# Performance work log

Measured on AMD Instinct MI355X. Metric: run time of the kernel, lower is better.

## Reference

```python
import jax, jax.numpy as jnp
import numpy as np

N, E, B = 10000, 20000, 400
ND, ED, D = 32, 16, 64


def setup_inputs() -> dict:
    key = jax.random.key(0)
    ks = jax.random.split(key, 32)

    def lin(k, out_d, in_d):
        kw, kb = jax.random.split(k)
        s = 1.0 / np.sqrt(in_d)
        return (jax.random.uniform(kw, (out_d, in_d), jnp.float32, -s, s),
                jax.random.uniform(kb, (out_d,), jnp.float32, -s, s))

    W_in, b_in = lin(ks[0], D, ND)
    W_e1, b_e1 = lin(ks[1], D, ED)
    W_e2, b_e2 = lin(ks[2], D * D, D)
    b_conv = jax.random.uniform(ks[3], (D,), jnp.float32, -1/8.0, 1/8.0)
    W_ih, b_ih = lin(ks[4], 3 * D, D)
    W_hh, b_hh = lin(ks[5], 3 * D, D)
    W_ih_l, b_ih_l = lin(ks[6], 4 * D, 2 * D)
    W_hh_l, b_hh_l = lin(ks[7], 4 * D, D)
    W_o1, b_o1 = lin(ks[8], D, 2 * D)
    W_o2, b_o2 = lin(ks[9], 1, D)

    x = jax.random.normal(ks[10], (N, ND), jnp.float32)
    edge_attr = jax.random.normal(ks[11], (E, ED), jnp.float32)
    edge_index = jax.random.randint(ks[12], (2, E), 0, N, jnp.int64)
    batch = jnp.sort(jax.random.randint(ks[13], (N,), 0, B, jnp.int64))

    return dict(x=x, edge_attr=edge_attr,
                W_in=W_in, b_in=b_in, W_e1=W_e1, b_e1=b_e1, W_e2=W_e2, b_e2=b_e2,
                b_conv=b_conv, W_ih=W_ih, b_ih=b_ih, W_hh=W_hh, b_hh=b_hh,
                W_ih_l=W_ih_l, b_ih_l=b_ih_l, W_hh_l=W_hh_l, b_hh_l=b_hh_l,
                W_o1=W_o1, b_o1=b_o1, W_o2=W_o2, b_o2=b_o2,
                edge_index=edge_index, batch=batch)


def reference(x, edge_attr, W_in, b_in, W_e1, b_e1, W_e2, b_e2, b_conv,
              W_ih, b_ih, W_hh, b_hh, W_ih_l, b_ih_l, W_hh_l, b_hh_l,
              W_o1, b_o1, W_o2, b_o2, edge_index, batch):
    src, dst = edge_index[0], edge_index[1]

    # in_linear
    out = jax.nn.relu(x @ W_in.T + b_in)            # [N, D]
    h = out                                          # GRU hidden (layer=1, seq=1)

    # edge-conditioned weights: MLP(edge_attr) -> [E, D, D]
    ew = (jax.nn.relu(edge_attr @ W_e1.T + b_e1) @ W_e2.T + b_e2).reshape(E, D, D)
    cnt = jnp.maximum(jax.ops.segment_sum(jnp.ones((E,), x.dtype), dst, N), 1.0)

    for _ in range(3):
        # NNConv: gather src nodes, per-edge matmul, scatter-mean to dst, + bias
        msg = jnp.einsum('ed,edf->ef', out[src], ew)                 # [E, D]
        agg = jax.ops.segment_sum(msg, dst, N) / cnt[:, None] + b_conv
        m = jax.nn.relu(agg)
        # GRU cell (torch gate order r, z, n)
        gi = m @ W_ih.T + b_ih
        gh = h @ W_hh.T + b_hh
        i_r, i_z, i_n = jnp.split(gi, 3, axis=-1)
        h_r, h_z, h_n = jnp.split(gh, 3, axis=-1)
        r = jax.nn.sigmoid(i_r + h_r)
        z = jax.nn.sigmoid(i_z + h_z)
        n = jnp.tanh(i_n + r * h_n)
        h = (1.0 - z) * n + z * h
        out = h

    # Set2Set pooling, processing_steps=3
    q_star = jnp.zeros((B, 2 * D), x.dtype)
    hl = jnp.zeros((B, D), x.dtype)
    cl = jnp.zeros((B, D), x.dtype)
    for _ in range(3):
        g = q_star @ W_ih_l.T + b_ih_l + hl @ W_hh_l.T + b_hh_l
        gi_, gf_, gg_, go_ = jnp.split(g, 4, axis=-1)   # torch order i,f,g,o
        cl = jax.nn.sigmoid(gf_) * cl + jax.nn.sigmoid(gi_) * jnp.tanh(gg_)
        hl = jax.nn.sigmoid(go_) * jnp.tanh(cl)
        q = hl                                           # [B, D]
        e = jnp.sum(out * q[batch], axis=-1)             # [N]
        mmax = jax.ops.segment_max(e, batch, B)
        a = jnp.exp(e - mmax[batch])
        a = a / jax.ops.segment_sum(a, batch, B)[batch]
        r_ = jax.ops.segment_sum(a[:, None] * out, batch, B)  # [B, D]
        q_star = jnp.concatenate([q, r_], axis=-1)

    o = jax.nn.relu(q_star @ W_o1.T + b_o1) @ W_o2.T + b_o2
    return o.reshape(-1)
```

## Files before the change

kernel.cpp:

```cpp
#include <hip/hip_runtime.h>
#include <math.h>


#define Nn 10000
#define Ee 20000
#define Bb 400
#define KSTEPS 130
#define S2S_CHUNK 1024

typedef __attribute__((ext_vector_type(8))) short bf16x8_t;
typedef __attribute__((ext_vector_type(4))) float f32x4_t;

__device__ __forceinline__ float sigmoidf_(float x) { return 1.f / (1.f + expf(-x)); }

__device__ __forceinline__ void split8(const float* p, bf16x8_t& Ahi_, bf16x8_t& Alo_) {
    union { bf16x8_t v; unsigned u[4]; } hi, lo;
#pragma unroll
    for (int ii = 0; ii < 4; ++ii) {
        float pa = p[2 * ii], pb = p[2 * ii + 1];
        unsigned ua = __float_as_uint(pa), ub = __float_as_uint(pb);
        hi.u[ii] = (ua >> 16) | (ub & 0xFFFF0000u);
        float la = pa - __uint_as_float(ua & 0xFFFF0000u);
        float lb = pb - __uint_as_float(ub & 0xFFFF0000u);
        lo.u[ii] = (__float_as_uint(la) >> 16) | (__float_as_uint(lb) & 0xFFFF0000u);
    }
    Ahi_ = hi.v; Alo_ = lo.v;
}

__global__ __launch_bounds__(256) void k_in_linear(const float* __restrict__ x,
                                                   const float* __restrict__ Win,
                                                   const float* __restrict__ bin,
                                                   float* __restrict__ out) {
    int idx = blockIdx.x * 256 + threadIdx.x;
    if (idx >= Nn * 64) return;
    int n = idx >> 6, j = idx & 63;
    const float* xr = x + n * 32;
    const float* w = Win + j * 32;
    float acc = bin[j];
#pragma unroll
    for (int k = 0; k < 32; ++k) acc += xr[k] * w[k];
    out[idx] = fmaxf(acc, 0.f);
}

__global__ __launch_bounds__(256) void k_edge_mlp1(const float* __restrict__ ea,
                                                   const float* __restrict__ W1,
                                                   const float* __restrict__ b1,
                                                   const int* __restrict__ epos,
                                                   float* __restrict__ eh) {
    int idx = blockIdx.x * 256 + threadIdx.x;
    if (idx >= Ee * 64) return;
    int e = idx >> 6, j = idx & 63;
    const float* ar = ea + e * 16;
    const float* w = W1 + j * 16;
    float acc = b1[j];
#pragma unroll
    for (int k = 0; k < 16; ++k) acc += ar[k] * w[k];
    eh[(size_t)epos[e] * 64 + j] = fmaxf(acc, 0.f);
}

__global__ __launch_bounds__(256) void k_make_Bfat(const float* __restrict__ W2,
                                                   const float* __restrict__ b2,
                                                   unsigned short* __restrict__ Bfat) {
    int idx = blockIdx.x * 256 + threadIdx.x;
    if (idx >= KSTEPS * 4096) return;
    int i  = idx & 7;
    int l  = (idx >> 3) & 63;
    int nq = (idx >> 9) & 3;
    int h  = (idx >> 11) & 1;
    int ks = idx >> 12;
    int kap = ks * 32 + (l >> 4) * 8 + i;
    int f = nq * 16 + (l & 15);
    float w;
    if (kap < 4096) {
        int q = kap >> 6, d = kap & 63;
        w = W2[(size_t)(d * 64 + f) * 64 + q];
    } else {
        int d = kap - 4096;
        w = b2[d * 64 + f];
    }
    unsigned u = __float_as_uint(w);
    unsigned short outv;
    if (h == 0) {
        outv = (unsigned short)(u >> 16);
    } else {
        float lo = w - __uint_as_float(u & 0xFFFF0000u);
        outv = (unsigned short)(__float_as_uint(lo) >> 16);
    }
    Bfat[idx] = outv;
}

__global__ __launch_bounds__(256) void k_make_Wg(const float* __restrict__ Wih,
                                                 const float* __restrict__ Whh,
                                                 unsigned short* __restrict__ Wg) {
    int idx = blockIdx.x * 256 + threadIdx.x;
    if (idx >= 4 * 2 * 16 * 64 * 8) return;
    int i  = idx & 7;
    int l  = (idx >> 3) & 63;
    int t  = (idx >> 9) & 15;
    int h  = (idx >> 13) & 1;
    int ks = idx >> 14;
    int k = ks * 32 + (l >> 4) * 8 + i;
    int u = t * 16 + (l & 15);
    int j = u & 63, part = u >> 6;
    float w = 0.f;
    if (part == 0) w = (k < 64) ? Wih[(size_t)j * 64 + k]          : Whh[(size_t)j * 64 + (k - 64)];
    if (part == 1) w = (k < 64) ? Wih[(size_t)(64 + j) * 64 + k]   : Whh[(size_t)(64 + j) * 64 + (k - 64)];
    if (part == 2) w = (k < 64) ? Wih[(size_t)(128 + j) * 64 + k]  : 0.f;
    if (part == 3) w = (k < 64) ? 0.f : Whh[(size_t)(128 + j) * 64 + (k - 64)];
    unsigned uu = __float_as_uint(w);
    unsigned short outv;
    if (h == 0) {
        outv = (unsigned short)(uu >> 16);
    } else {
        float lo = w - __uint_as_float(uu & 0xFFFF0000u);
        outv = (unsigned short)(__float_as_uint(lo) >> 16);
    }
    Wg[idx] = outv;
}

__global__ __launch_bounds__(256) void k_count_deg(const int* __restrict__ ei,
                                                   int* __restrict__ deg) {
    int e = blockIdx.x * 256 + threadIdx.x;
    if (e >= Ee) return;
    atomicAdd(&deg[ei[Ee + e]], 1);
}

__global__ __launch_bounds__(256) void k_scan_nodes(const int* __restrict__ deg,
                                                    int* __restrict__ rowptr,
                                                    int* __restrict__ wptr) {
    __shared__ int part[256];
    int t = threadIdx.x;
    const int PER = (Nn + 255) / 256;
    int b0 = t * PER;
    int s = 0;
    for (int i = 0; i < PER; ++i) {
        int idx = b0 + i;
        if (idx < Nn) s += deg[idx];
    }
    part[t] = s;
    __syncthreads();
    for (int o = 1; o < 256; o <<= 1) {
        int u = (t >= o) ? part[t - o] : 0;
        __syncthreads();
        part[t] += u;
        __syncthreads();
    }
    int run = part[t] - s;
    for (int i = 0; i < PER; ++i) {
        int idx = b0 + i;
        if (idx < Nn) {
            rowptr[idx] = run;
            wptr[idx] = run;
            run += deg[idx];
        }
    }
    if (t == 255) rowptr[Nn] = run;
}

__global__ __launch_bounds__(256) void k_sort_edges(const int* __restrict__ ei,
                                                    int* __restrict__ wptr,
                                                    int* __restrict__ srcs,
                                                    int* __restrict__ epos) {
    int e = blockIdx.x * 256 + threadIdx.x;
    if (e >= Ee) return;
    int d = ei[Ee + e];
    int p = atomicAdd(&wptr[d], 1);
    srcs[p] = ei[e];
    epos[e] = p;
}

__global__ __launch_bounds__(256, 3) void k_msg_mfma(const float* __restrict__ out,
                                                     const float* __restrict__ eh,
                                                     const unsigned short* __restrict__ Bfat,
                                                     const int* __restrict__ srcs_g,
                                                     float* __restrict__ msgbuf,
                                                     int nsplit) {
    __shared__ float ehs[128][20];
    __shared__ int srcs[128];
    int tid = threadIdx.x;
    int ebase = blockIdx.x * 128;
    int ksplit = blockIdx.y;

    int ks0 = (KSTEPS * ksplit) / nsplit;
    int ks1 = (KSTEPS * (ksplit + 1)) / nsplit;
    int q0 = ks0 >> 1;
    int qn = ((min(ks1, 128) - 1) >> 1) - q0 + 1;

    {
        int el = tid >> 1, seg = tid & 1;
        int eg = ebase + el;
        bool v = eg < Ee;
        if (seg == 0) srcs[el] = v ? srcs_g[eg] : 0;
        const float* erow = eh + (size_t)eg * 64;
        for (int j = seg; j < qn; j += 2)
            ehs[el][j] = v ? erow[q0 + j] : 0.f;
    }
    __syncthreads();

    int lane = tid & 63;
    int wtile = tid >> 6;
    int m16 = lane & 15;
    int g = lane >> 4;
    int erA = wtile * 32 + m16;
    int erB = erA + 16;

    float a0[2][8], a1[2][8];
    {
        const float* rA = out + (size_t)srcs[erA] * 64;
        const float* rB = out + (size_t)srcs[erB] * 64;
        float4 v0, v1;
        v0 = *(const float4*)(rA + g * 8);      v1 = *(const float4*)(rA + g * 8 + 4);
        a0[0][0]=v0.x; a0[0][1]=v0.y; a0[0][2]=v0.z; a0[0][3]=v0.w;
        a0[0][4]=v1.x; a0[0][5]=v1.y; a0[0][6]=v1.z; a0[0][7]=v1.w;
        v0 = *(const float4*)(rA + 32 + g * 8); v1 = *(const float4*)(rA + 36 + g * 8);
        a1[0][0]=v0.x; a1[0][1]=v0.y; a1[0][2]=v0.z; a1[0][3]=v0.w;
        a1[0][4]=v1.x; a1[0][5]=v1.y; a1[0][6]=v1.z; a1[0][7]=v1.w;
        v0 = *(const float4*)(rB + g * 8);      v1 = *(const float4*)(rB + g * 8 + 4);
        a0[1][0]=v0.x; a0[1][1]=v0.y; a0[1][2]=v0.z; a0[1][3]=v0.w;
        a0[1][4]=v1.x; a0[1][5]=v1.y; a0[1][6]=v1.z; a0[1][7]=v1.w;
        v0 = *(const float4*)(rB + 32 + g * 8); v1 = *(const float4*)(rB + 36 + g * 8);
        a1[1][0]=v0.x; a1[1][1]=v0.y; a1[1][2]=v0.z; a1[1][3]=v0.w;
        a1[1][4]=v1.x; a1[1][5]=v1.y; a1[1][6]=v1.z; a1[1][7]=v1.w;
    }

    f32x4_t acc[2][4];
#pragma unroll
    for (int t = 0; t < 2; ++t)
#pragma unroll
        for (int nq = 0; nq < 4; ++nq) acc[t][nq] = (f32x4_t){0.f, 0.f, 0.f, 0.f};

    auto body = [&](int ks, const float (&Av)[2][8], float qA, float qB) {
        const unsigned short* bstep = Bfat + (size_t)ks * 4096;
        bf16x8_t bhi[4], blo[4];
#pragma unroll
        for (int nq = 0; nq < 4; ++nq) {
            bhi[nq] = *(const bf16x8_t*)(bstep + ((size_t)(nq * 64 + lane)) * 8);
            blo[nq] = *(const bf16x8_t*)(bstep + ((size_t)((4 + nq) * 64 + lane)) * 8);
        }
        float pA[8], pB[8];
#pragma unroll
        for (int i = 0; i < 8; ++i) { pA[i] = Av[0][i] * qA; pB[i] = Av[1][i] * qB; }
        bf16x8_t AhiA, AloA, AhiB, AloB;
        split8(pA, AhiA, AloA);
        split8(pB, AhiB, AloB);
#pragma unroll
        for (int nq = 0; nq < 4; ++nq) {
            acc[0][nq] = __builtin_amdgcn_mfma_f32_16x16x32_bf16(AhiA, bhi[nq], acc[0][nq], 0, 0, 0);
            acc[0][nq] = __builtin_amdgcn_mfma_f32_16x16x32_bf16(AhiA, blo[nq], acc[0][nq], 0, 0, 0);
            acc[0][nq] = __builtin_amdgcn_mfma_f32_16x16x32_bf16(AloA, bhi[nq], acc[0][nq], 0, 0, 0);
            acc[1][nq] = __builtin_amdgcn_mfma_f32_16x16x32_bf16(AhiB, bhi[nq], acc[1][nq], 0, 0, 0);
            acc[1][nq] = __builtin_amdgcn_mfma_f32_16x16x32_bf16(AhiB, blo[nq], acc[1][nq], 0, 0, 0);
            acc[1][nq] = __builtin_amdgcn_mfma_f32_16x16x32_bf16(AloB, bhi[nq], acc[1][nq], 0, 0, 0);
        }
    };

    for (int kp = ks0 & ~1; kp < ks1; kp += 2) {
        float qA = 1.f, qB = 1.f;
        if (kp < 128) {
            int qi = (kp >> 1) - q0;
            if (qi >= 0) { qA = ehs[erA][qi]; qB = ehs[erB][qi]; }
        }
        if (kp >= ks0)    body(kp,     a0, qA, qB);
        if (kp + 1 < ks1) body(kp + 1, a1, qA, qB);
    }

#pragma unroll
    for (int t = 0; t < 2; ++t) {
#pragma unroll
        for (int r = 0; r < 4; ++r) {
            int el = wtile * 32 + t * 16 + g * 4 + r;
            int eg = ebase + el;
            if (eg >= Ee) continue;
            float* mrow = msgbuf + ((size_t)ksplit * Ee + eg) * 64 + m16;
#pragma unroll
            for (int nq = 0; nq < 4; ++nq)
                mrow[nq * 16] = acc[t][nq][r];
        }
    }
}

__global__ __launch_bounds__(256) void k_gru_mfma(const float* __restrict__ msgbuf,
                                                  const int* __restrict__ rowptr,
                                                  const float* __restrict__ bconv,
                                                  const unsigned short* __restrict__ Wg,
                                                  const float* __restrict__ bih,
                                                  const float* __restrict__ bhh,
                                                  float* __restrict__ out,
                                                  int nsplit) {
    __shared__ float ms[64][68];
    __shared__ float hs[64][68];
    int tid = threadIdx.x;
    int nbase = blockIdx.x * 64;

    {
        int nl = tid >> 2, seg = tid & 3;
        int ng = nbase + nl;
        bool v = ng < Nn;
        int p0 = v ? rowptr[ng] : 0;
        int p1 = v ? rowptr[ng + 1] : 0;
        int dg = p1 - p0;
        float rc = 1.f / (float)(dg < 1 ? 1 : dg);
        float s[16];
#pragma unroll
        for (int i = 0; i < 16; ++i) s[i] = 0.f;
        for (int sp = 0; sp < nsplit; ++sp) {
            const float* mb = msgbuf + (size_t)sp * Ee * 64;
            for (int p = p0; p < p1; ++p) {
                const float* mrow = mb + (size_t)p * 64 + seg * 16;
#pragma unroll
                for (int c4 = 0; c4 < 4; ++c4) {
                    float4 t4 = *(const float4*)(mrow + c4 * 4);
                    s[c4 * 4 + 0] += t4.x;
                    s[c4 * 4 + 1] += t4.y;
                    s[c4 * 4 + 2] += t4.z;
                    s[c4 * 4 + 3] += t4.w;
                }
            }
        }
        const float* hrow = out + (size_t)ng * 64 + seg * 16;
        float4 z = make_float4(0.f, 0.f, 0.f, 0.f);
#pragma unroll
        for (int c4 = 0; c4 < 4; ++c4) {
            int col = seg * 16 + c4 * 4;
            float4 hv = v ? *(const float4*)(hrow + c4 * 4) : z;
            ms[nl][col + 0] = fmaxf(s[c4 * 4 + 0] * rc + bconv[col + 0], 0.f);
            ms[nl][col + 1] = fmaxf(s[c4 * 4 + 1] * rc + bconv[col + 1], 0.f);
            ms[nl][col + 2] = fmaxf(s[c4 * 4 + 2] * rc + bconv[col + 2], 0.f);
            ms[nl][col + 3] = fmaxf(s[c4 * 4 + 3] * rc + bconv[col + 3], 0.f);
            *(float4*)&hs[nl][col] = hv;
        }
    }
    __syncthreads();

    int lane = tid & 63;
    int wtile = tid >> 6;
    int m16 = lane & 15;
    int g = lane >> 4;
    int er = wtile * 16 + m16;

    f32x4_t acc[16];
#pragma unroll
    for (int t = 0; t < 16; ++t) acc[t] = (f32x4_t){0.f, 0.f, 0.f, 0.f};

#pragma unroll
    for (int ks = 0; ks < 4; ++ks) {
        const float* src = (ks < 2) ? &ms[er][ks * 32 + g * 8]
                                    : &hs[er][(ks - 2) * 32 + g * 8];
        float p[8];
#pragma unroll
        for (int ii = 0; ii < 8; ++ii) p[ii] = src[ii];
        bf16x8_t Ahi, Alo;
        split8(p, Ahi, Alo);
        const unsigned short* bstep = Wg + (size_t)ks * (2 * 16 * 512);
#pragma unroll
        for (int t = 0; t < 16; ++t) {
            bf16x8_t bhi = *(const bf16x8_t*)(bstep + ((size_t)t * 64 + lane) * 8);
            bf16x8_t blo = *(const bf16x8_t*)(bstep + ((size_t)(16 + t) * 64 + lane) * 8);
            acc[t] = __builtin_amdgcn_mfma_f32_16x16x32_bf16(Ahi, bhi, acc[t], 0, 0, 0);
            acc[t] = __builtin_amdgcn_mfma_f32_16x16x32_bf16(Ahi, blo, acc[t], 0, 0, 0);
            acc[t] = __builtin_amdgcn_mfma_f32_16x16x32_bf16(Alo, bhi, acc[t], 0, 0, 0);
        }
    }

#pragma unroll
    for (int t2 = 0; t2 < 4; ++t2) {
        int jj = t2 * 16 + m16;
        float br = bih[jj] + bhh[jj];
        float bz = bih[64 + jj] + bhh[64 + jj];
        float bin_ = bih[128 + jj];
        float bhn = bhh[128 + jj];
#pragma unroll
        for (int r = 0; r < 4; ++r) {
            int nl2 = wtile * 16 + g * 4 + r;
            int ng2 = nbase + nl2;
            if (ng2 >= Nn) continue;
            float rg = sigmoidf_(acc[t2][r] + br);
            float z  = sigmoidf_(acc[4 + t2][r] + bz);
            float nn = tanhf(acc[8 + t2][r] + bin_ + rg * (acc[12 + t2][r] + bhn));
            float hv = hs[nl2][jj];
            out[(size_t)ng2 * 64 + jj] = (1.f - z) * nn + z * hv;
        }
    }
}

__global__ __launch_bounds__(256) void k_count_batch(const int* __restrict__ batch,
                                                     int* __restrict__ bcount) {
    int n = blockIdx.x * 256 + threadIdx.x;
    if (n >= Nn) return;
    atomicAdd(&bcount[batch[n]], 1);
}

__global__ __launch_bounds__(64) void k_scan_batch(const int* __restrict__ bcount,
                                                   int* __restrict__ bstart) {
    int lane = threadIdx.x;
    const int PER = (Bb + 63) / 64;
    int base = lane * PER;
    int v[PER];
    int s = 0;
#pragma unroll
    for (int i = 0; i < PER; ++i) {
        int idx = base + i;
        int c = (idx < Bb) ? bcount[idx] : 0;
        v[i] = s;
        s += c;
    }
    int inc = s;
#pragma unroll
    for (int o = 1; o < 64; o <<= 1) {
        int t = __shfl_up(inc, o, 64);
        if (lane >= o) inc += t;
    }
    int excl = inc - s;
    int total = __shfl(inc, 63, 64);
#pragma unroll
    for (int i = 0; i < PER; ++i) {
        int idx = base + i;
        if (idx < Bb) bstart[idx] = excl + v[i];
    }
    if (lane == 63) bstart[Bb] = total;
}

__device__ __forceinline__ float block_reduce_max_(float v, float* red, int tid) {
#pragma unroll
    for (int o = 32; o; o >>= 1) v = fmaxf(v, __shfl_xor(v, o, 64));
    if ((tid & 63) == 0) red[tid >> 6] = v;
    __syncthreads();
    float r = fmaxf(fmaxf(red[0], red[1]), fmaxf(red[2], red[3]));
    __syncthreads();
    return r;
}
__device__ __forceinline__ float block_reduce_sum_(float v, float* red, int tid) {
#pragma unroll
    for (int o = 32; o; o >>= 1) v += __shfl_xor(v, o, 64);
    if ((tid & 63) == 0) red[tid >> 6] = v;
    __syncthreads();
    float r = (red[0] + red[1]) + (red[2] + red[3]);
    __syncthreads();
    return r;
}

__global__ __launch_bounds__(256) void k_set2set(const float* __restrict__ out,
                                                 const int* __restrict__ bstart,
                                                 const float* __restrict__ Wil,
                                                 const float* __restrict__ bil,
                                                 const float* __restrict__ Whl,
                                                 const float* __restrict__ bhl,
                                                 const float* __restrict__ Wo1,
                                                 const float* __restrict__ bo1,
                                                 const float* __restrict__ Wo2,
                                                 const float* __restrict__ bo2,
                                                 float* __restrict__ outp) {
    __shared__ float qs[128];
    __shared__ float hs2[64];
    __shared__ float cs[64];
    __shared__ float g_lds[256];
    __shared__ float e_lds[S2S_CHUNK];
    __shared__ float red[4];
    __shared__ float rpart[4][64];

    int b = blockIdx.x, tid = threadIdx.x;
    int lane = tid & 63, wv = tid >> 6;
    int s = bstart[b], eend = bstart[b + 1];
    int cntb = eend - s;

    if (tid < 128) qs[tid] = 0.f;
    if (tid < 64) { hs2[tid] = 0.f; cs[tid] = 0.f; }
    __syncthreads();

    for (int step = 0; step < 3; ++step) {
        {
            int u = tid;
            float acc = bil[u] + bhl[u];
            const float4* wi = (const float4*)(Wil + (size_t)u * 128);
#pragma unroll
            for (int k4 = 0; k4 < 32; ++k4) {
                float4 w = wi[k4];
                acc += qs[k4 * 4 + 0] * w.x + qs[k4 * 4 + 1] * w.y +
                       qs[k4 * 4 + 2] * w.z + qs[k4 * 4 + 3] * w.w;
            }
            const float4* wh = (const float4*)(Whl + (size_t)u * 64);
#pragma unroll
            for (int k4 = 0; k4 < 16; ++k4) {
                float4 w = wh[k4];
                acc += hs2[k4 * 4 + 0] * w.x + hs2[k4 * 4 + 1] * w.y +
                       hs2[k4 * 4 + 2] * w.z + hs2[k4 * 4 + 3] * w.w;
            }
            g_lds[u] = acc;
        }
        __syncthreads();
        if (tid < 64) {
            float c = sigmoidf_(g_lds[64 + tid]) * cs[tid] +
                      sigmoidf_(g_lds[tid]) * tanhf(g_lds[128 + tid]);
            cs[tid] = c;
            float h = sigmoidf_(g_lds[192 + tid]) * tanhf(c);
            hs2[tid] = h;
            qs[tid] = h;
        }
        __syncthreads();

        float gmax = -INFINITY, gsum = 0.f, racc = 0.f;
        for (int c0 = s; c0 < eend; c0 += S2S_CHUNK) {
            int clen = min(S2S_CHUNK, eend - c0);
            for (int i = tid; i < clen; i += 256) {
                const float4* orow = (const float4*)(out + (size_t)(c0 + i) * 64);
                float a0 = 0.f, a1 = 0.f, a2 = 0.f, a3 = 0.f;
#pragma unroll
                for (int k4 = 0; k4 < 16; k4 += 4) {
                    float4 o0 = orow[k4], o1 = orow[k4 + 1], o2 = orow[k4 + 2], o3 = orow[k4 + 3];
                    a0 += o0.x * qs[k4 * 4 + 0]  + o0.y * qs[k4 * 4 + 1]  + o0.z * qs[k4 * 4 + 2]  + o0.w * qs[k4 * 4 + 3];
                    a1 += o1.x * qs[k4 * 4 + 4]  + o1.y * qs[k4 * 4 + 5]  + o1.z * qs[k4 * 4 + 6]  + o1.w * qs[k4 * 4 + 7];
                    a2 += o2.x * qs[k4 * 4 + 8]  + o2.y * qs[k4 * 4 + 9]  + o2.z * qs[k4 * 4 + 10] + o2.w * qs[k4 * 4 + 11];
                    a3 += o3.x * qs[k4 * 4 + 12] + o3.y * qs[k4 * 4 + 13] + o3.z * qs[k4 * 4 + 14] + o3.w * qs[k4 * 4 + 15];
                }
                e_lds[i] = (a0 + a1) + (a2 + a3);
            }
            __syncthreads();
            float m = -INFINITY;
            for (int i = tid; i < clen; i += 256) m = fmaxf(m, e_lds[i]);
            float cmax = block_reduce_max_(m, red, tid);
            float nm = fmaxf(gmax, cmax);
            float scale = expf(gmax - nm);
            gsum *= scale; racc *= scale;
            float lsum = 0.f;
            for (int i = tid; i < clen; i += 256) {
                float av = expf(e_lds[i] - nm);
                e_lds[i] = av;
                lsum += av;
            }
            gsum += block_reduce_sum_(lsum, red, tid);
            for (int i = wv; i < clen; i += 4)
                racc += e_lds[i] * out[(size_t)(c0 + i) * 64 + lane];
            gmax = nm;
            __syncthreads();
        }
        rpart[wv][lane] = racc;
        __syncthreads();
        if (tid < 64) {
            float r = (rpart[0][tid] + rpart[1][tid]) + (rpart[2][tid] + rpart[3][tid]);
            qs[64 + tid] = (cntb > 0) ? r / gsum : 0.f;
        }
        __syncthreads();
    }

    if (tid < 64) {
        float acc = bo1[tid];
        const float4* w = (const float4*)(Wo1 + (size_t)tid * 128);
#pragma unroll
        for (int k4 = 0; k4 < 32; ++k4) {
            float4 wv4 = w[k4];
            acc += qs[k4 * 4 + 0] * wv4.x + qs[k4 * 4 + 1] * wv4.y +
                   qs[k4 * 4 + 2] * wv4.z + qs[k4 * 4 + 3] * wv4.w;
        }
        acc = fmaxf(acc, 0.f);
        float t = acc * Wo2[tid];
#pragma unroll
        for (int o = 32; o; o >>= 1) t += __shfl_xor(t, o, 64);
        if (tid == 0) outp[b] = t + bo2[0];
    }
}

extern "C" void kernel_launch(void* const* d_in, const int* in_sizes, int n_in,
                              void* d_out, int out_size, void* d_ws, size_t ws_size,
                              hipStream_t stream) {
    const float* x        = (const float*)d_in[0];
    const float* ea       = (const float*)d_in[1];
    const float* W_in     = (const float*)d_in[2];
    const float* b_in     = (const float*)d_in[3];
    const float* W_e1     = (const float*)d_in[4];
    const float* b_e1     = (const float*)d_in[5];
    const float* W_e2     = (const float*)d_in[6];
    const float* b_e2     = (const float*)d_in[7];
    const float* b_conv   = (const float*)d_in[8];
    const float* W_ih     = (const float*)d_in[9];
    const float* b_ih     = (const float*)d_in[10];
    const float* W_hh     = (const float*)d_in[11];
    const float* b_hh     = (const float*)d_in[12];
    const float* W_ih_l   = (const float*)d_in[13];
    const float* b_ih_l   = (const float*)d_in[14];
    const float* W_hh_l   = (const float*)d_in[15];
    const float* b_hh_l   = (const float*)d_in[16];
    const float* W_o1     = (const float*)d_in[17];
    const float* b_o1     = (const float*)d_in[18];
    const float* W_o2     = (const float*)d_in[19];
    const float* b_o2     = (const float*)d_in[20];
    const int*   ei       = (const int*)d_in[21];
    const int*   batch    = (const int*)d_in[22];
    float* outp = (float*)d_out;

    char* base = (char*)d_ws;
    size_t off = 0;
    auto carve = [&](size_t bytes) -> void* {
        void* p = base + off;
        off = (off + bytes + 255) & ~(size_t)255;
        return p;
    };

    int ns = 4;
    float *out, *msgbuf, *eh;
    unsigned short *Bfat, *Wg;
    int *srcs, *epos, *rowptr, *wptr, *deg, *bcount, *bstart;
    for (;; ns >>= 1) {
        off = 0;
        out    = (float*)carve((size_t)Nn * 64 * 4);
        msgbuf = (float*)carve((size_t)ns * Ee * 64 * 4);
        eh     = (float*)carve((size_t)Ee * 64 * 4);
        Bfat   = (unsigned short*)carve((size_t)KSTEPS * 4096 * 2);
        Wg     = (unsigned short*)carve((size_t)4 * 2 * 16 * 64 * 8 * 2);
        srcs   = (int*)carve((size_t)Ee * 4);
        epos   = (int*)carve((size_t)Ee * 4);
        rowptr = (int*)carve((size_t)(Nn + 1) * 4);
        wptr   = (int*)carve((size_t)Nn * 4);
        deg    = (int*)carve((size_t)Nn * 4);
        bcount = (int*)carve((size_t)Bb * 4);
        bstart = (int*)carve((size_t)(Bb + 1) * 4);
        if (off <= ws_size || ns == 1) break;
    }
    if (off > ws_size) return;

    hipMemsetAsync(deg, 0, (size_t)Nn * 4, stream);
    hipMemsetAsync(bcount, 0, (size_t)Bb * 4, stream);

    k_count_deg<<<(Ee + 255) / 256, 256, 0, stream>>>(ei, deg);
    k_scan_nodes<<<1, 256, 0, stream>>>(deg, rowptr, wptr);
    k_sort_edges<<<(Ee + 255) / 256, 256, 0, stream>>>(ei, wptr, srcs, epos);

    k_in_linear<<<(Nn * 64) / 256, 256, 0, stream>>>(x, W_in, b_in, out);
    k_edge_mlp1<<<(Ee * 64) / 256, 256, 0, stream>>>(ea, W_e1, b_e1, epos, eh);
    k_make_Bfat<<<(KSTEPS * 4096) / 256, 256, 0, stream>>>(W_e2, b_e2, Bfat);
    k_make_Wg<<<(4 * 2 * 16 * 64 * 8) / 256, 256, 0, stream>>>(W_ih, W_hh, Wg);
    k_count_batch<<<(Nn + 255) / 256, 256, 0, stream>>>(batch, bcount);
    k_scan_batch<<<1, 64, 0, stream>>>(bcount, bstart);

    int eblocks = (Ee + 127) / 128;
    int nblocks = (Nn + 63) / 64;
    for (int it = 0; it < 3; ++it) {
        k_msg_mfma<<<dim3(eblocks, ns), 256, 0, stream>>>(out, eh, Bfat, srcs, msgbuf, ns);
        k_gru_mfma<<<nblocks, 256, 0, stream>>>(msgbuf, rowptr, b_conv, Wg, b_ih, b_hh, out, ns);
    }

    k_set2set<<<Bb, 256, 0, stream>>>(out, bstart, W_ih_l, b_ih_l, W_hh_l, b_hh_l,
                                      W_o1, b_o1, W_o2, b_o2, outp);
}
```

Before: 340.2 us.

## Merge setup kernels and double-buffer B fragment loads in message kernel

Merges the in-linear, Bfat and Wg preparation kernels into one fill launch, and combines degree/batch counting and their scans into paired kernels, cutting the number of small serial launches. Separately, the message MFMA kernel now prefetches the next k-step's B fragments into registers while the current step computes, and its occupancy hint in launch_bounds is removed. The prefetch raises register pressure, and dropping the occupancy hint may let the compiler lower occupancy.

Result: faster. 332.8 us (-2.2%).

```diff
diff --git a/kernel.cpp b/kernel.cpp
--- a/kernel.cpp
+++ b/kernel.cpp
@@ -7,6 +7,10 @@
 #define Bb 400
 #define KSTEPS 130
 #define S2S_CHUNK 1024
+
+#define FILL_A (Nn * 64)
+#define FILL_B (KSTEPS * 4096)
+#define FILL_C (4 * 2 * 16 * 64 * 8)
 
 typedef __attribute__((ext_vector_type(8))) short bf16x8_t;
 typedef __attribute__((ext_vector_type(4))) float f32x4_t;
@@ -27,19 +31,80 @@
     Ahi_ = hi.v; Alo_ = lo.v;
 }
 
-__global__ __launch_bounds__(256) void k_in_linear(const float* __restrict__ x,
-                                                   const float* __restrict__ Win,
-                                                   const float* __restrict__ bin,
-                                                   float* __restrict__ out) {
+__global__ __launch_bounds__(256) void k_fill(const float* __restrict__ x,
+                                              const float* __restrict__ Win,
+                                              const float* __restrict__ bin,
+                                              const float* __restrict__ W2,
+                                              const float* __restrict__ b2,
+                                              const float* __restrict__ Wih,
+                                              const float* __restrict__ Whh,
+                                              float* __restrict__ out,
+                                              unsigned short* __restrict__ Bfat,
+                                              unsigned short* __restrict__ Wg) {
     int idx = blockIdx.x * 256 + threadIdx.x;
-    if (idx >= Nn * 64) return;
-    int n = idx >> 6, j = idx & 63;
-    const float* xr = x + n * 32;
-    const float* w = Win + j * 32;
-    float acc = bin[j];
-#pragma unroll
-    for (int k = 0; k < 32; ++k) acc += xr[k] * w[k];
-    out[idx] = fmaxf(acc, 0.f);
+    if (idx < FILL_A) {
+        int n = idx >> 6, j = idx & 63;
+        const float* xr = x + n * 32;
+        const float* w = Win + j * 32;
+        float acc = bin[j];
+#pragma unroll
+        for (int k = 0; k < 32; ++k) acc += xr[k] * w[k];
+        out[idx] = fmaxf(acc, 0.f);
+        return;
+    }
+    idx -= FILL_A;
+    if (idx < FILL_B) {
+        int i  = idx & 7;
+        int l  = (idx >> 3) & 63;
+        int nq = (idx >> 9) & 3;
+        int h  = (idx >> 11) & 1;
+        int ks = idx >> 12;
+        int kap = ks * 32 + (l >> 4) * 8 + i;
+        int f = nq * 16 + (l & 15);
+        float w;
+        if (kap < 4096) {
+            int q = kap >> 6, d = kap & 63;
+            w = W2[(size_t)(d * 64 + f) * 64 + q];
+        } else {
+            int d = kap - 4096;
+            w = b2[d * 64 + f];
+        }
+        unsigned u = __float_as_uint(w);
+        unsigned short outv;
+        if (h == 0) {
+            outv = (unsigned short)(u >> 16);
+        } else {
+            float lo = w - __uint_as_float(u & 0xFFFF0000u);
+            outv = (unsigned short)(__float_as_uint(lo) >> 16);
+        }
+        Bfat[idx] = outv;
+        return;
+    }
+    idx -= FILL_B;
+    if (idx < FILL_C) {
+        int i  = idx & 7;
+        int l  = (idx >> 3) & 63;
+        int t  = (idx >> 9) & 15;
+        int h  = (idx >> 13) & 1;
+        int ks = idx >> 14;
+        int k = ks * 32 + (l >> 4) * 8 + i;
+        int u = t * 16 + (l & 15);
+        int j = u & 63, part = u >> 6;
+        float w = 0.f;
+        if (part == 0) w = (k < 64) ? Wih[(size_t)j * 64 + k]          : Whh[(size_t)j * 64 + (k - 64)];
+        if (part == 1) w = (k < 64) ? Wih[(size_t)(64 + j) * 64 + k]   : Whh[(size_t)(64 + j) * 64 + (k - 64)];
+        if (part == 2) w = (k < 64) ? Wih[(size_t)(128 + j) * 64 + k]  : 0.f;
+        if (part == 3) w = (k < 64) ? 0.f : Whh[(size_t)(128 + j) * 64 + (k - 64)];
+        unsigned uu = __float_as_uint(w);
+        unsigned short outv;
+        if (h == 0) {
+            outv = (unsigned short)(uu >> 16);
+        } else {
+            float lo = w - __uint_as_float(uu & 0xFFFF0000u);
+            outv = (unsigned short)(__float_as_uint(lo) >> 16);
+        }
+        Wg[idx] = outv;
+    }
 }
 
 __global__ __launch_bounds__(256) void k_edge_mlp1(const float* __restrict__ ea,
@@ -58,103 +123,79 @@
     eh[(size_t)epos[e] * 64 + j] = fmaxf(acc, 0.f);
 }
 
-__global__ __launch_bounds__(256) void k_make_Bfat(const float* __restrict__ W2,
-                                                   const float* __restrict__ b2,
-                                                   unsigned short* __restrict__ Bfat) {
+__global__ __launch_bounds__(256) void k_prep_count(const int* __restrict__ ei,
+                                                    const int* __restrict__ batch,
+                                                    int* __restrict__ deg,
+                                                    int* __restrict__ bcount) {
     int idx = blockIdx.x * 256 + threadIdx.x;
-    if (idx >= KSTEPS * 4096) return;
-    int i  = idx & 7;
-    int l  = (idx >> 3) & 63;
-    int nq = (idx >> 9) & 3;
-    int h  = (idx >> 11) & 1;
-    int ks = idx >> 12;
-    int kap = ks * 32 + (l >> 4) * 8 + i;
-    int f = nq * 16 + (l & 15);
-    float w;
-    if (kap < 4096) {
-        int q = kap >> 6, d = kap & 63;
-        w = W2[(size_t)(d * 64 + f) * 64 + q];
-    } else {
-        int d = kap - 4096;
-        w = b2[d * 64 + f];
-    }
-    unsigned u = __float_as_uint(w);
-    unsigned short outv;
-    if (h == 0) {
-        outv = (unsigned short)(u >> 16);
-    } else {
-        float lo = w - __uint_as_float(u & 0xFFFF0000u);
-        outv = (unsigned short)(__float_as_uint(lo) >> 16);
-    }
-    Bfat[idx] = outv;
-}
-
-__global__ __launch_bounds__(256) void k_make_Wg(const float* __restrict__ Wih,
-                                                 const float* __restrict__ Whh,
-                                                 unsigned short* __restrict__ Wg) {
-    int idx = blockIdx.x * 256 + threadIdx.x;
-    if (idx >= 4 * 2 * 16 * 64 * 8) return;
-    int i  = idx & 7;
-    int l  = (idx >> 3) & 63;
-    int t  = (idx >> 9) & 15;
-    int h  = (idx >> 13) & 1;
-    int ks = idx >> 14;
-    int k = ks * 32 + (l >> 4) * 8 + i;
-    int u = t * 16 + (l & 15);
-    int j = u & 63, part = u >> 6;
-    float w = 0.f;
-    if (part == 0) w = (k < 64) ? Wih[(size_t)j * 64 + k]          : Whh[(size_t)j * 64 + (k - 64)];
-    if (part == 1) w = (k < 64) ? Wih[(size_t)(64 + j) * 64 + k]   : Whh[(size_t)(64 + j) * 64 + (k - 64)];
-    if (part == 2) w = (k < 64) ? Wih[(size_t)(128 + j) * 64 + k]  : 0.f;
-    if (part == 3) w = (k < 64) ? 0.f : Whh[(size_t)(128 + j) * 64 + (k - 64)];
-    unsigned uu = __float_as_uint(w);
-    unsigned short outv;
-    if (h == 0) {
-        outv = (unsigned short)(uu >> 16);
-    } else {
-        float lo = w - __uint_as_float(uu & 0xFFFF0000u);
-        outv = (unsigned short)(__float_as_uint(lo) >> 16);
-    }
-    Wg[idx] = outv;
-}
-
-__global__ __launch_bounds__(256) void k_count_deg(const int* __restrict__ ei,
-                                                   int* __restrict__ deg) {
-    int e = blockIdx.x * 256 + threadIdx.x;
-    if (e >= Ee) return;
-    atomicAdd(&deg[ei[Ee + e]], 1);
-}
-
-__global__ __launch_bounds__(256) void k_scan_nodes(const int* __restrict__ deg,
-                                                    int* __restrict__ rowptr,
-                                                    int* __restrict__ wptr) {
-    __shared__ int part[256];
-    int t = threadIdx.x;
-    const int PER = (Nn + 255) / 256;
-    int b0 = t * PER;
-    int s = 0;
-    for (int i = 0; i < PER; ++i) {
-        int idx = b0 + i;
-        if (idx < Nn) s += deg[idx];
-    }
-    part[t] = s;
-    __syncthreads();
-    for (int o = 1; o < 256; o <<= 1) {
-        int u = (t >= o) ? part[t - o] : 0;
+    if (idx < Ee) {
+        atomicAdd(&deg[ei[Ee + idx]], 1);
+    } else if (idx < Ee + Nn) {
+        atomicAdd(&bcount[batch[idx - Ee]], 1);
+    }
+}
+
+__global__ __launch_bounds__(256) void k_prep_scan(const int* __restrict__ deg,
+                                                   const int* __restrict__ bcount,
+                                                   int* __restrict__ rowptr,
+                                                   int* __restrict__ wptr,
+                                                   int* __restrict__ bstart) {
+    if (blockIdx.x == 0) {
+        __shared__ int part[256];
+        int t = threadIdx.x;
+        const int PER = (Nn + 255) / 256;
+        int b0 = t * PER;
+        int s = 0;
+        for (int i = 0; i < PER; ++i) {
+            int idx = b0 + i;
+            if (idx < Nn) s += deg[idx];
+        }
+        part[t] = s;
         __syncthreads();
-        part[t] += u;
-        __syncthreads();
-    }
-    int run = part[t] - s;
-    for (int i = 0; i < PER; ++i) {
-        int idx = b0 + i;
-        if (idx < Nn) {
-            rowptr[idx] = run;
-            wptr[idx] = run;
-            run += deg[idx];
-        }
-    }
-    if (t == 255) rowptr[Nn] = run;
+        for (int o = 1; o < 256; o <<= 1) {
+            int u = (t >= o) ? part[t - o] : 0;
+            __syncthreads();
+            part[t] += u;
+            __syncthreads();
+        }
+        int run = part[t] - s;
+        for (int i = 0; i < PER; ++i) {
+            int idx = b0 + i;
+            if (idx < Nn) {
+                rowptr[idx] = run;
+                wptr[idx] = run;
+                run += deg[idx];
+            }
+        }
+        if (t == 255) rowptr[Nn] = run;
+    } else if (threadIdx.x < 64) {
+        int lane = threadIdx.x;
+        const int PER = (Bb + 63) / 64;
+        int base = lane * PER;
+        int v[PER];
+        int s = 0;
+#pragma unroll
+        for (int i = 0; i < PER; ++i) {
+            int idx = base + i;
+            int c = (idx < Bb) ? bcount[idx] : 0;
+            v[i] = s;
+            s += c;
+        }
+        int inc = s;
+#pragma unroll
+        for (int o = 1; o < 64; o <<= 1) {
+            int t = __shfl_up(inc, o, 64);
+            if (lane >= o) inc += t;
+        }
+        int excl = inc - s;
+        int total = __shfl(inc, 63, 64);
+#pragma unroll
+        for (int i = 0; i < PER; ++i) {
+            int idx = base + i;
+            if (idx < Bb) bstart[idx] = excl + v[i];
+        }
+        if (lane == 63) bstart[Bb] = total;
+    }
 }
 
 __global__ __launch_bounds__(256) void k_sort_edges(const int* __restrict__ ei,
@@ -169,12 +210,12 @@
     epos[e] = p;
 }
 
-__global__ __launch_bounds__(256, 3) void k_msg_mfma(const float* __restrict__ out,
-                                                     const float* __restrict__ eh,
-                                                     const unsigned short* __restrict__ Bfat,
-                                                     const int* __restrict__ srcs_g,
-                                                     float* __restrict__ msgbuf,
-                                                     int nsplit) {
+__global__ __launch_bounds__(256) void k_msg_mfma(const float* __restrict__ out,
+                                                  const float* __restrict__ eh,
+                                                  const unsigned short* __restrict__ Bfat,
+                                                  const int* __restrict__ srcs_g,
+                                                  float* __restrict__ msgbuf,
+                                                  int nsplit) {
     __shared__ float ehs[128][20];
     __shared__ int srcs[128];
     int tid = threadIdx.x;
@@ -229,14 +270,16 @@
 #pragma unroll
         for (int nq = 0; nq < 4; ++nq) acc[t][nq] = (f32x4_t){0.f, 0.f, 0.f, 0.f};
 
-    auto body = [&](int ks, const float (&Av)[2][8], float qA, float qB) {
+    auto loadB = [&](int ks, bf16x8_t (&bh)[4], bf16x8_t (&bl)[4]) {
         const unsigned short* bstep = Bfat + (size_t)ks * 4096;
-        bf16x8_t bhi[4], blo[4];
 #pragma unroll
         for (int nq = 0; nq < 4; ++nq) {
-            bhi[nq] = *(const bf16x8_t*)(bstep + ((size_t)(nq * 64 + lane)) * 8);
-            blo[nq] = *(const bf16x8_t*)(bstep + ((size_t)((4 + nq) * 64 + lane)) * 8);
-        }
+            bh[nq] = *(const bf16x8_t*)(bstep + ((size_t)(nq * 64 + lane)) * 8);
+            bl[nq] = *(const bf16x8_t*)(bstep + ((size_t)((4 + nq) * 64 + lane)) * 8);
+        }
+    };
+    auto compute = [&](const float (&Av)[2][8], float qA, float qB,
+                       const bf16x8_t (&bh)[4], const bf16x8_t (&bl)[4]) {
         float pA[8], pB[8];
 #pragma unroll
         for (int i = 0; i < 8; ++i) { pA[i] = Av[0][i] * qA; pB[i] = Av[1][i] * qB; }
@@ -245,23 +288,29 @@
         split8(pB, AhiB, AloB);
 #pragma unroll
         for (int nq = 0; nq < 4; ++nq) {
-            acc[0][nq] = __builtin_amdgcn_mfma_f32_16x16x32_bf16(AhiA, bhi[nq], acc[0][nq], 0, 0, 0);
-            acc[0][nq] = __builtin_amdgcn_mfma_f32_16x16x32_bf16(AhiA, blo[nq], acc[0][nq], 0, 0, 0);
-            acc[0][nq] = __builtin_amdgcn_mfma_f32_16x16x32_bf16(AloA, bhi[nq], acc[0][nq], 0, 0, 0);
-            acc[1][nq] = __builtin_amdgcn_mfma_f32_16x16x32_bf16(AhiB, bhi[nq], acc[1][nq], 0, 0, 0);
-            acc[1][nq] = __builtin_amdgcn_mfma_f32_16x16x32_bf16(AhiB, blo[nq], acc[1][nq], 0, 0, 0);
-            acc[1][nq] = __builtin_amdgcn_mfma_f32_16x16x32_bf16(AloB, bhi[nq], acc[1][nq], 0, 0, 0);
+            acc[0][nq] = __builtin_amdgcn_mfma_f32_16x16x32_bf16(AhiA, bh[nq], acc[0][nq], 0, 0, 0);
+            acc[0][nq] = __builtin_amdgcn_mfma_f32_16x16x32_bf16(AhiA, bl[nq], acc[0][nq], 0, 0, 0);
+            acc[0][nq] = __builtin_amdgcn_mfma_f32_16x16x32_bf16(AloA, bh[nq], acc[0][nq], 0, 0, 0);
+            acc[1][nq] = __builtin_amdgcn_mfma_f32_16x16x32_bf16(AhiB, bh[nq], acc[1][nq], 0, 0, 0);
+            acc[1][nq] = __builtin_amdgcn_mfma_f32_16x16x32_bf16(AhiB, bl[nq], acc[1][nq], 0, 0, 0);
+            acc[1][nq] = __builtin_amdgcn_mfma_f32_16x16x32_bf16(AloB, bh[nq], acc[1][nq], 0, 0, 0);
         }
     };
 
-    for (int kp = ks0 & ~1; kp < ks1; kp += 2) {
+    bf16x8_t bEh[4], bEl[4], bOh[4], bOl[4];
+    int kp0 = ks0 & ~1;
+    loadB(kp0, bEh, bEl);
+    for (int kp = kp0; kp < ks1; kp += 2) {
+        bool hasOdd = (kp + 1 < ks1);
+        if (hasOdd) loadB(kp + 1, bOh, bOl);
         float qA = 1.f, qB = 1.f;
         if (kp < 128) {
             int qi = (kp >> 1) - q0;
             if (qi >= 0) { qA = ehs[erA][qi]; qB = ehs[erB][qi]; }
         }
-        if (kp >= ks0)    body(kp,     a0, qA, qB);
-        if (kp + 1 < ks1) body(kp + 1, a1, qA, qB);
+        if (kp >= ks0) compute(a0, qA, qB, bEh, bEl);
+        if (kp + 2 < ks1) loadB(kp + 2, bEh, bEl);
+        if (hasOdd) compute(a1, qA, qB, bOh, bOl);
     }
 
 #pragma unroll
@@ -381,43 +430,6 @@
             out[(size_t)ng2 * 64 + jj] = (1.f - z) * nn + z * hv;
         }
     }
-}
-
-__global__ __launch_bounds__(256) void k_count_batch(const int* __restrict__ batch,
-                                                     int* __restrict__ bcount) {
-    int n = blockIdx.x * 256 + threadIdx.x;
-    if (n >= Nn) return;
-    atomicAdd(&bcount[batch[n]], 1);
-}
-
-__global__ __launch_bounds__(64) void k_scan_batch(const int* __restrict__ bcount,
-                                                   int* __restrict__ bstart) {
-    int lane = threadIdx.x;
-    const int PER = (Bb + 63) / 64;
-    int base = lane * PER;
-    int v[PER];
-    int s = 0;
-#pragma unroll
-    for (int i = 0; i < PER; ++i) {
-        int idx = base + i;
-        int c = (idx < Bb) ? bcount[idx] : 0;
-        v[i] = s;
-        s += c;
-    }
-    int inc = s;
-#pragma unroll
-    for (int o = 1; o < 64; o <<= 1) {
-        int t = __shfl_up(inc, o, 64);
-        if (lane >= o) inc += t;
-    }
-    int excl = inc - s;
-    int total = __shfl(inc, 63, 64);
-#pragma unroll
-    for (int i = 0; i < PER; ++i) {
-        int idx = base + i;
-        if (idx < Bb) bstart[idx] = excl + v[i];
-    }
-    if (lane == 63) bstart[Bb] = total;
 }
 
 __device__ __forceinline__ float block_reduce_max_(float v, float* red, int tid) {
@@ -620,16 +632,13 @@
     hipMemsetAsync(deg, 0, (size_t)Nn * 4, stream);
     hipMemsetAsync(bcount, 0, (size_t)Bb * 4, stream);
 
-    k_count_deg<<<(Ee + 255) / 256, 256, 0, stream>>>(ei, deg);
-    k_scan_nodes<<<1, 256, 0, stream>>>(deg, rowptr, wptr);
+    k_prep_count<<<(Ee + Nn + 255) / 256, 256, 0, stream>>>(ei, batch, deg, bcount);
+    k_prep_scan<<<2, 256, 0, stream>>>(deg, bcount, rowptr, wptr, bstart);
     k_sort_edges<<<(Ee + 255) / 256, 256, 0, stream>>>(ei, wptr, srcs, epos);
 
-    k_in_linear<<<(Nn * 64) / 256, 256, 0, stream>>>(x, W_in, b_in, out);
+    k_fill<<<(FILL_A + FILL_B + FILL_C + 255) / 256, 256, 0, stream>>>(
+        x, W_in, b_in, W_e2, b_e2, W_ih, W_hh, out, Bfat, Wg);
     k_edge_mlp1<<<(Ee * 64) / 256, 256, 0, stream>>>(ea, W_e1, b_e1, epos, eh);
-    k_make_Bfat<<<(KSTEPS * 4096) / 256, 256, 0, stream>>>(W_e2, b_e2, Bfat);
-    k_make_Wg<<<(4 * 2 * 16 * 64 * 8) / 256, 256, 0, stream>>>(W_ih, W_hh, Wg);
-    k_count_batch<<<(Nn + 255) / 256, 256, 0, stream>>>(batch, bcount);
-    k_scan_batch<<<1, 64, 0, stream>>>(bcount, bstart);
 
     int eblocks = (Ee + 127) / 128;
     int nblocks = (Nn + 63) / 64;
```
